# Kernel tuning notes

Measured on AMD Instinct MI355X. Metric: run time of the kernel, lower is better.

Reference implementation:

```python
import jax, jax.numpy as jnp
import numpy as np
from jax import lax

EPS = 1e-8
QB = 127.0  # 2**(8-1) - 1
LN_EPS = 1e-5

B, S, E, D = 32, 4096, 64, 32


def _ste(x, q):
    return x + lax.stop_gradient(q - x)


def _bitlinear(x, w, b):
    # BitLinear158b: ternary absmean weight quant + 8-bit absmax activation quant (STE)
    beta = jnp.maximum(jnp.mean(jnp.abs(w)), EPS)
    wq = jnp.clip(jnp.round(w / beta), -1.0, 1.0) * beta
    gamma = QB / jnp.maximum(jnp.max(jnp.abs(x), axis=-1, keepdims=True), EPS)
    xq = jnp.clip(jnp.round(x * gamma), -(QB + 1.0), QB) / gamma
    return _ste(x, xq) @ _ste(w, wq).T + b


def _layernorm(x, g, b):
    m = jnp.mean(x, axis=-1, keepdims=True)
    v = jnp.mean(jnp.square(x - m), axis=-1, keepdims=True)
    return (x - m) * lax.rsqrt(v + LN_EPS) * g + b


def _conv3x3(x, w, b):
    y = lax.conv_general_dilated(x, w, (1, 1), 'SAME',
                                 dimension_numbers=('NCHW', 'OIHW', 'NCHW'))
    return y + b.reshape(1, -1, 1, 1)


def _gelu(x):
    return jax.nn.gelu(x, approximate=False)


def setup_inputs() -> dict:
    key = jax.random.key(0)
    ks = jax.random.split(key, 20)
    d = {
        'x': jax.random.normal(ks[0], (B, S, E), jnp.float32),
        'interact2': jax.random.normal(ks[1], (B, D, D), jnp.float32),
        'qw': jax.random.normal(ks[2], (E, E), jnp.float32) * 0.05,
        'qb': jnp.zeros((E,), jnp.float32),
        'kw': jax.random.normal(ks[3], (E, E), jnp.float32) * 0.05,
        'kb': jnp.zeros((E,), jnp.float32),
        'vw': jax.random.normal(ks[4], (E, E), jnp.float32) * 0.05,
        'vb': jnp.zeros((E,), jnp.float32),
        'f1w': jax.random.normal(ks[5], (E, E), jnp.float32) * 0.05,
        'f1b': jnp.zeros((E,), jnp.float32),
        'f2w': jax.random.normal(ks[6], (E, E), jnp.float32) * 0.05,
        'f2b': jnp.zeros((E,), jnp.float32),
        'c1w': jax.random.normal(ks[7], (1, 1, 3, 3), jnp.float32) * 0.2,
        'c1b': jnp.zeros((1,), jnp.float32),
        'c2w': jax.random.normal(ks[8], (1, 1, 3, 3), jnp.float32) * 0.2,
        'c2b': jnp.zeros((1,), jnp.float32),
        'c3w': jax.random.normal(ks[9], (1, 1, 3, 3), jnp.float32) * 0.2,
        'c3b': jnp.zeros((1,), jnp.float32),
        'ln1g': jnp.ones((E,), jnp.float32), 'ln1b': jnp.zeros((E,), jnp.float32),
        'ln2g': jnp.ones((E,), jnp.float32), 'ln2b': jnp.zeros((E,), jnp.float32),
        'ln3g': jnp.ones((E,), jnp.float32), 'ln3b': jnp.zeros((E,), jnp.float32),
        'ln4g': jnp.ones((E,), jnp.float32), 'ln4b': jnp.zeros((E,), jnp.float32),
    }
    return d


def reference(x, interact2, qw, qb, kw, kb, vw, vb, f1w, f1b, f2w, f2b,
              c1w, c1b, c2w, c2b, c3w, c3b,
              ln1g, ln1b, ln2g, ln2b, ln3g, ln3b, ln4g, ln4b):
    residual1 = x
    b, s, e = x.shape
    xn = _layernorm(x, ln1g, ln1b)
    # NOTE: .view(B, E, S) is a raw reinterpret of the (B,S,E) buffer, not a transpose
    q = _bitlinear(xn, qw, qb).reshape(b, e, s)
    k = _bitlinear(xn, kw, kb).reshape(b, e, s)
    v = _bitlinear(xn, vw, vb).reshape(b, e, s)

    it = interact2[:, None, :, :]
    it = jax.image.resize(it, (b, 1, 64, 64), method='linear')  # align_corners=False
    it = _gelu(_conv3x3(it, c1w, c1b))  # dropout4: identity (eval)
    it = _gelu(_conv3x3(it, c2w, c2b))
    it = _gelu(_conv3x3(it, c3w, c3b))
    it = it[:, 0]  # (B, 64, 64)

    scale = jnp.sqrt(jnp.float32(e))
    scores = jnp.einsum('bes,bfs->bef', q, k) / scale + it  # (B,E,E)
    attn = jax.nn.softmax(scores, axis=-1)
    out = jnp.einsum('bef,bfs->bes', attn, v)  # (B,E,S)
    out = jnp.transpose(out, (0, 2, 1)).reshape(b, s, e)
    out = out - xn  # dropout: identity (eval)
    out = _layernorm(out, ln2g, ln2b)
    residual2 = out + residual1
    out = _layernorm(out + residual1, ln3g, ln3b)
    out = _gelu(_bitlinear(out, f1w, f1b))
    out = _layernorm(out, ln4g, ln4b)
    out = _bitlinear(out, f2w, f2b)
    return out + residual2
```

## Files before the change

### kernel.cpp

```cpp
#include <hip/hip_runtime.h>

#define EPSQ 1e-8f
#define QBC  127.0f
#define LNE  1e-5f

#if defined(__has_builtin)
#  if __has_builtin(__builtin_amdgcn_sdot4)
#    define SDOT4(a,b,c) __builtin_amdgcn_sdot4((a),(b),(c),false)
#  endif
#endif
#ifndef SDOT4
__device__ __forceinline__ int sdot4_sw(int a, int b, int c){
  c += ((a<<24)>>24) * ((b<<24)>>24);
  c += ((a<<16)>>24) * ((b<<16)>>24);
  c += ((a<< 8)>>24) * ((b<< 8)>>24);
  c += ( a>>24     ) * ( b>>24     );
  return c;
}
#  define SDOT4(a,b,c) sdot4_sw((a),(b),(c))
#endif

constexpr size_t OFF_WPK  = 0;
constexpr size_t OFF_BETA = 20480;
constexpr size_t OFF_IG   = 20544;
constexpr size_t OFF_XN   = OFF_IG + 524288;
constexpr size_t OFF_Q    = OFF_XN + 33554432;
constexpr size_t OFF_K    = OFF_Q  + 16777216;
constexpr size_t OFF_V    = OFF_K  + 16777216;
constexpr size_t OFF_SC   = OFF_V  + 16777216;
constexpr size_t OFF_AT   = OFF_SC + 524288;

__device__ __forceinline__ float gelu_f(float v){
  return 0.5f * v * (1.0f + erff(v * 0.70710678118654752f));
}
__device__ __forceinline__ int pack4(float q0, float q1, float q2, float q3){
  return ((int)q0 & 255) | (((int)q1 & 255) << 8) | (((int)q2 & 255) << 16) | (((int)q3 & 255) << 24);
}

__global__ __launch_bounds__(256) void k_prep(
    const float* qw, const float* kw, const float* vw, const float* f1w, const float* f2w,
    const float* it2, const float* c1w, const float* c1b, const float* c2w, const float* c2b,
    const float* c3w, const float* c3b, int* __restrict__ wpk, float* __restrict__ beta5,
    float* __restrict__ sco){
  __shared__ float smem[1024 + 2*64*65];
  int t = threadIdx.x;
  if (blockIdx.x < 5){
    int m = blockIdx.x;
    const float* w = (m==0)?qw:(m==1)?kw:(m==2)?vw:(m==3)?f1w:f2w;
    float* red = smem;
    float s = 0.f;
    for (int i = t; i < 4096; i += 256) s += fabsf(w[i]);
    red[t] = s; __syncthreads();
    for (int o = 128; o > 0; o >>= 1){ if (t < o) red[t] += red[t+o]; __syncthreads(); }
    float beta = fmaxf(red[0] * (1.0f/4096.0f), EPSQ);
    if (t == 0) beta5[m] = beta;
    int* dst = wpk + m*1024;
    for (int idx = t; idx < 1024; idx += 256){
      int row = idx >> 4, kp = idx & 15;
      int v = 0;
      #pragma unroll
      for (int j = 0; j < 4; j++){
        float q = rintf(w[row*64 + kp*4 + j] / beta);
        q = fminf(fmaxf(q, -1.f), 1.f);
        v |= ((int)q & 255) << (8*j);
      }
      dst[idx] = v;
    }
  } else {
    int b = blockIdx.x - 5;
    float* in32 = smem;
    float (*Aa)[65] = (float(*)[65])(smem + 1024);
    float (*Bb)[65] = (float(*)[65])(smem + 1024 + 64*65);
    for (int i = t; i < 1024; i += 256) in32[i] = it2[b*1024 + i];
    __syncthreads();
    for (int p = t; p < 4096; p += 256){
      int i = p >> 6, j = p & 63;
      float si = 0.5f*i - 0.25f, fi = floorf(si), wi = si - fi;
      int i0 = min(max((int)fi, 0), 31), i1 = min(max((int)fi + 1, 0), 31);
      float sj = 0.5f*j - 0.25f, fj = floorf(sj), wj = sj - fj;
      int j0 = min(max((int)fj, 0), 31), j1 = min(max((int)fj + 1, 0), 31);
      float v00 = in32[i0*32+j0], v01 = in32[i0*32+j1];
      float v10 = in32[i1*32+j0], v11 = in32[i1*32+j1];
      Aa[i][j] = (1.f-wi)*((1.f-wj)*v00 + wj*v01) + wi*((1.f-wj)*v10 + wj*v11);
    }
    __syncthreads();
    {
      float w9[9]; for (int q2=0;q2<9;q2++) w9[q2]=c1w[q2]; float bb = c1b[0];
      for (int p = t; p < 4096; p += 256){
        int i = p>>6, j = p&63; float s = bb;
        #pragma unroll
        for (int di=-1; di<=1; di++)
          #pragma unroll
          for (int dj=-1; dj<=1; dj++){
            int ii=i+di, jj=j+dj;
            if (ii>=0 && ii<64 && jj>=0 && jj<64) s += w9[(di+1)*3+dj+1]*Aa[ii][jj];
          }
        Bb[i][j] = gelu_f(s);
      }
    }
    __syncthreads();
    {
      float w9[9]; for (int q2=0;q2<9;q2++) w9[q2]=c2w[q2]; float bb = c2b[0];
      for (int p = t; p < 4096; p += 256){
        int i = p>>6, j = p&63; float s = bb;
        #pragma unroll
        for (int di=-1; di<=1; di++)
          #pragma unroll
          for (int dj=-1; dj<=1; dj++){
            int ii=i+di, jj=j+dj;
            if (ii>=0 && ii<64 && jj>=0 && jj<64) s += w9[(di+1)*3+dj+1]*Bb[ii][jj];
          }
        Aa[i][j] = gelu_f(s);
      }
    }
    __syncthreads();
    {
      float w9[9]; for (int q2=0;q2<9;q2++) w9[q2]=c3w[q2]; float bb = c3b[0];
      for (int p = t; p < 4096; p += 256){
        int i = p>>6, j = p&63; float s = bb;
        #pragma unroll
        for (int di=-1; di<=1; di++)
          #pragma unroll
          for (int dj=-1; dj<=1; dj++){
            int ii=i+di, jj=j+dj;
            if (ii>=0 && ii<64 && jj>=0 && jj<64) s += w9[(di+1)*3+dj+1]*Aa[ii][jj];
          }
        sco[b*4096 + p] = gelu_f(s);
      }
    }
  }
}

__global__ __launch_bounds__(256,4) void k_qkv(const float* __restrict__ x,
    const float* __restrict__ ln1g, const float* __restrict__ ln1b,
    const int* __restrict__ wpk, float* __restrict__ xn, float* __restrict__ ig,
    short* __restrict__ q16, short* __restrict__ k16, short* __restrict__ v16){
  __shared__ int Wp[3][64][17];
  __shared__ int Xp[64][17];
  int t = threadIdx.x;
  for (int i = t; i < 3072; i += 256){
    int m = i >> 10, rem = i & 1023;
    Wp[m][rem>>4][rem&15] = wpk[i];
  }
  int c = t >> 2, g = t & 3;
  long n = (long)blockIdx.x * 64 + c;
  const float* xr = x + n*64 + g*16;
  float xv[16];
  #pragma unroll
  for (int i4 = 0; i4 < 4; i4++){
    float4 f = ((const float4*)xr)[i4];
    xv[4*i4+0]=f.x; xv[4*i4+1]=f.y; xv[4*i4+2]=f.z; xv[4*i4+3]=f.w;
  }
  float s = 0.f;
  #pragma unroll
  for (int i = 0; i < 16; i++) s += xv[i];
  s += __shfl_xor(s,1); s += __shfl_xor(s,2);
  float mean = s * (1.0f/64.0f);
  float vs = 0.f;
  #pragma unroll
  for (int i = 0; i < 16; i++){ float dd = xv[i]-mean; vs += dd*dd; }
  vs += __shfl_xor(vs,1); vs += __shfl_xor(vs,2);
  float rs = rsqrtf(vs*(1.0f/64.0f) + LNE);
  float xnv[16]; float amax = 0.f;
  #pragma unroll
  for (int i = 0; i < 16; i++){
    float u = (xv[i]-mean)*rs*ln1g[g*16+i] + ln1b[g*16+i];
    xnv[i] = u; amax = fmaxf(amax, fabsf(u));
  }
  float* xnp = xn + n*64 + g*16;
  #pragma unroll
  for (int i4 = 0; i4 < 4; i4++)
    ((float4*)xnp)[i4] = make_float4(xnv[4*i4],xnv[4*i4+1],xnv[4*i4+2],xnv[4*i4+3]);
  amax = fmaxf(amax, __shfl_xor(amax,1)); amax = fmaxf(amax, __shfl_xor(amax,2));
  float am = fmaxf(amax, EPSQ);
  float gamma = QBC / am;
  if (g == 0) ig[n] = am * (1.0f/QBC);
  #pragma unroll
  for (int i4 = 0; i4 < 4; i4++){
    float q0 = fminf(fmaxf(rintf(xnv[4*i4+0]*gamma), -128.f), 127.f);
    float q1 = fminf(fmaxf(rintf(xnv[4*i4+1]*gamma), -128.f), 127.f);
    float q2 = fminf(fmaxf(rintf(xnv[4*i4+2]*gamma), -128.f), 127.f);
    float q3 = fminf(fmaxf(rintf(xnv[4*i4+3]*gamma), -128.f), 127.f);
    Xp[c][g*4+i4] = pack4(q0,q1,q2,q3);
  }
  __syncthreads();

  int r0 = (t >> 4) << 2, c0 = (t & 15) << 2;
  #pragma unroll
  for (int m = 0; m < 3; m++){
    int acc[4][4] = {};
    #pragma unroll
    for (int kp = 0; kp < 16; kp++){
      int av[4], bv[4];
      #pragma unroll
      for (int i = 0; i < 4; i++) av[i] = Xp[r0+i][kp];
      #pragma unroll
      for (int j = 0; j < 4; j++) bv[j] = Wp[m][c0+j][kp];
      #pragma unroll
      for (int i = 0; i < 4; i++)
        #pragma unroll
        for (int j = 0; j < 4; j++)
          acc[i][j] = SDOT4(av[i], bv[j], acc[i][j]);
    }
    short* op = ((m==0)?q16:(m==1)?k16:v16) + (long)blockIdx.x*4096;
    #pragma unroll
    for (int i = 0; i < 4; i++){
      short4 s4;
      s4.x = (short)acc[i][0]; s4.y = (short)acc[i][1];
      s4.z = (short)acc[i][2]; s4.w = (short)acc[i][3];
      *(short4*)&op[(r0+i)*64 + c0] = s4;
    }
  }
}

__global__ __launch_bounds__(256,4) void k_qk(
    const short* __restrict__ q16, const short* __restrict__ k16,
    const float* __restrict__ ig, const float* __restrict__ beta5,
    const float* __restrict__ qbias, const float* __restrict__ kbias,
    float* __restrict__ sco){
  __shared__ float Qs[64][68];
  __shared__ float Kt[64][68];
  __shared__ float qbs[64], kbs[64];
  int t = threadIdx.x;
  int b = blockIdx.x >> 4, ch = blockIdx.x & 15;
  int c = t >> 2, g = t & 3;
  int r0 = (t >> 4) << 2, c0 = (t & 15) << 2;
  if (t < 64){ qbs[t] = qbias[t]; kbs[t] = kbias[t]; }
  float bq = beta5[0], bk = beta5[1];
  const short* qbase = q16 + (long)b*262144 + (long)c*4096;
  const short* kbase = k16 + (long)b*262144 + (long)c*4096;
  float acc[4][4] = {};
  for (int sub = 0; sub < 4; sub++){
    int t0 = ch*256 + sub*64 + g*16;
    int4 qa = *(const int4*)(qbase + t0);
    int4 qb2 = *(const int4*)(qbase + t0 + 8);
    int4 ka = *(const int4*)(kbase + t0);
    int4 kb2 = *(const int4*)(kbase + t0 + 8);
    float sgi = ig[b*4096 + c*64 + ch*4 + sub];
    float sq = bq * sgi, sk = bk * sgi;
    __syncthreads();
    int qi[8] = {qa.x,qa.y,qa.z,qa.w,qb2.x,qb2.y,qb2.z,qb2.w};
    int ki[8] = {ka.x,ka.y,ka.z,ka.w,kb2.x,kb2.y,kb2.z,kb2.w};
    #pragma unroll
    for (int w2 = 0; w2 < 8; w2++){
      int e0 = g*16 + 2*w2, e1 = e0 + 1;
      Qs[c][e0] = (float)((qi[w2]<<16)>>16)*sq + qbs[e0];
      Qs[c][e1] = (float)( qi[w2]>>16      )*sq + qbs[e1];
      Kt[e0][c] = (float)((ki[w2]<<16)>>16)*sk + kbs[e0];
      Kt[e1][c] = (float)( ki[w2]>>16      )*sk + kbs[e1];
    }
    __syncthreads();
    for (int k4 = 0; k4 < 64; k4 += 4){
      float4 a[4], bv[4];
      #pragma unroll
      for (int i = 0; i < 4; i++) a[i] = *(const float4*)&Qs[r0+i][k4];
      #pragma unroll
      for (int kk = 0; kk < 4; kk++) bv[kk] = *(const float4*)&Kt[k4+kk][c0];
      #pragma unroll
      for (int i = 0; i < 4; i++){
        const float* ap = (const float*)&a[i];
        #pragma unroll
        for (int kk = 0; kk < 4; kk++){
          float av = ap[kk];
          acc[i][0] = fmaf(av, bv[kk].x, acc[i][0]);
          acc[i][1] = fmaf(av, bv[kk].y, acc[i][1]);
          acc[i][2] = fmaf(av, bv[kk].z, acc[i][2]);
          acc[i][3] = fmaf(av, bv[kk].w, acc[i][3]);
        }
      }
    }
  }
  float* sc = sco + b*4096;
  #pragma unroll
  for (int i = 0; i < 4; i++)
    #pragma unroll
    for (int j = 0; j < 4; j++)
      atomicAdd(&sc[(r0+i)*64 + c0 + j], acc[i][j]*0.125f);
}

__global__ __launch_bounds__(256) void k_smax(const float* __restrict__ sco, float* __restrict__ at){
  int row = blockIdx.x*4 + (threadIdx.x >> 6);
  int lane = threadIdx.x & 63;
  float v = sco[row*64 + lane];
  float m = v;
  #pragma unroll
  for (int o = 1; o < 64; o <<= 1) m = fmaxf(m, __shfl_xor(m, o));
  float e = expf(v - m);
  float s = e;
  #pragma unroll
  for (int o = 1; o < 64; o <<= 1) s += __shfl_xor(s, o);
  at[row*64 + lane] = e / s;
}

__global__ __launch_bounds__(256,3) void k_epi(const float* __restrict__ x,
    const short* __restrict__ v16, const float* __restrict__ at,
    const float* __restrict__ xn, const float* __restrict__ ig,
    const float* __restrict__ beta5, const int* __restrict__ wpk,
    const float* ln2g, const float* ln2b, const float* ln3g, const float* ln3b,
    const float* ln4g, const float* ln4b, const float* __restrict__ vbias,
    const float* f1b, const float* f2b, float* __restrict__ out){
  __shared__ float B1[64][68];
  __shared__ float B2[64][68];
  __shared__ int Wp[2][64][17];
  __shared__ int Xp[64][17];
  __shared__ float gam1[64], gam2[64];
  int t = threadIdx.x;
  int b = blockIdx.x >> 6;
  int s0 = (blockIdx.x & 63) << 6;
  float bv_ = beta5[2];
  for (int i = t; i < 4096; i += 256){
    int r = i >> 6, cc = i & 63;
    B1[r][cc] = at[b*4096 + i];
    float sv = bv_ * ig[b*4096 + r*64 + (s0 >> 6)];
    B2[r][cc] = (float)v16[(long)b*262144 + (long)r*4096 + s0 + cc] * sv + vbias[cc];
  }
  for (int i = t; i < 2048; i += 256){
    int m = i >> 10, rem = i & 1023;
    Wp[m][rem>>4][rem&15] = wpk[(3+m)*1024 + rem];
  }
  __syncthreads();
  int r0 = (t >> 4) << 2, c0 = (t & 15) << 2;
  float acc[4][4] = {};
  for (int k4 = 0; k4 < 64; k4 += 4){
    float4 a[4], bv[4];
    #pragma unroll
    for (int i = 0; i < 4; i++) a[i] = *(const float4*)&B1[r0+i][k4];
    #pragma unroll
    for (int kk = 0; kk < 4; kk++) bv[kk] = *(const float4*)&B2[k4+kk][c0];
    #pragma unroll
    for (int i = 0; i < 4; i++){
      const float* ap = (const float*)&a[i];
      #pragma unroll
      for (int kk = 0; kk < 4; kk++){
        float av = ap[kk];
        acc[i][0] = fmaf(av, bv[kk].x, acc[i][0]);
        acc[i][1] = fmaf(av, bv[kk].y, acc[i][1]);
        acc[i][2] = fmaf(av, bv[kk].z, acc[i][2]);
        acc[i][3] = fmaf(av, bv[kk].w, acc[i][3]);
      }
    }
  }
  __syncthreads();
  #pragma unroll
  for (int i = 0; i < 4; i++)
    #pragma unroll
    for (int j = 0; j < 4; j++) B1[c0+j][r0+i] = acc[i][j];
  __syncthreads();
  int c = t >> 2, g = t & 3;
  long n = (long)b*4096 + s0 + c;
  float d[16];
  #pragma unroll
  for (int i4 = 0; i4 < 4; i4++){
    float4 f = *(const float4*)&B1[c][g*16 + 4*i4];
    d[4*i4+0]=f.x; d[4*i4+1]=f.y; d[4*i4+2]=f.z; d[4*i4+3]=f.w;
  }
  const float* xnp = xn + n*64 + g*16;
  #pragma unroll
  for (int i4 = 0; i4 < 4; i4++){
    float4 f = ((const float4*)xnp)[i4];
    d[4*i4+0]-=f.x; d[4*i4+1]-=f.y; d[4*i4+2]-=f.z; d[4*i4+3]-=f.w;
  }
  float s = 0.f;
  #pragma unroll
  for (int i = 0; i < 16; i++) s += d[i];
  s += __shfl_xor(s,1); s += __shfl_xor(s,2);
  float mean = s*(1.0f/64.0f);
  float vs = 0.f;
  #pragma unroll
  for (int i = 0; i < 16; i++){ float dd = d[i]-mean; vs += dd*dd; }
  vs += __shfl_xor(vs,1); vs += __shfl_xor(vs,2);
  float rs = rsqrtf(vs*(1.0f/64.0f) + LNE);
  const float* xp = x + n*64 + g*16;
  float r2[16];
  #pragma unroll
  for (int i4 = 0; i4 < 4; i4++){
    float4 xf = ((const float4*)xp)[i4];
    float xa[4] = {xf.x, xf.y, xf.z, xf.w};
    #pragma unroll
    for (int q2 = 0; q2 < 4; q2++){
      int i = 4*i4+q2;
      float t2 = (d[i]-mean)*rs*ln2g[g*16+i] + ln2b[g*16+i];
      r2[i] = t2 + xa[q2];
    }
  }
  #pragma unroll
  for (int i4 = 0; i4 < 4; i4++)
    *(float4*)&B2[c][g*16+4*i4] = make_float4(r2[4*i4],r2[4*i4+1],r2[4*i4+2],r2[4*i4+3]);
  s = 0.f;
  #pragma unroll
  for (int i = 0; i < 16; i++) s += r2[i];
  s += __shfl_xor(s,1); s += __shfl_xor(s,2);
  float mean3 = s*(1.0f/64.0f);
  vs = 0.f;
  #pragma unroll
  for (int i = 0; i < 16; i++){ float dd = r2[i]-mean3; vs += dd*dd; }
  vs += __shfl_xor(vs,1); vs += __shfl_xor(vs,2);
  float rs3 = rsqrtf(vs*(1.0f/64.0f) + LNE);
  float u16v[16]; float amax = 0.f;
  #pragma unroll
  for (int i = 0; i < 16; i++){
    float u = (r2[i]-mean3)*rs3*ln3g[g*16+i] + ln3b[g*16+i];
    u16v[i] = u; amax = fmaxf(amax, fabsf(u));
  }
  amax = fmaxf(amax, __shfl_xor(amax,1)); amax = fmaxf(amax, __shfl_xor(amax,2));
  float gamma = QBC / fmaxf(amax, EPSQ);
  #pragma unroll
  for (int i4 = 0; i4 < 4; i4++){
    float q0 = fminf(fmaxf(rintf(u16v[4*i4+0]*gamma), -128.f), 127.f);
    float q1 = fminf(fmaxf(rintf(u16v[4*i4+1]*gamma), -128.f), 127.f);
    float q2 = fminf(fmaxf(rintf(u16v[4*i4+2]*gamma), -128.f), 127.f);
    float q3 = fminf(fmaxf(rintf(u16v[4*i4+3]*gamma), -128.f), 127.f);
    Xp[c][g*4+i4] = pack4(q0,q1,q2,q3);
  }
  if (g == 0) gam1[c] = gamma;
  __syncthreads();
  int ac2[4][4] = {};
  #pragma unroll
  for (int kp = 0; kp < 16; kp++){
    int av[4], bv2[4];
    #pragma unroll
    for (int i = 0; i < 4; i++) av[i] = Xp[r0+i][kp];
    #pragma unroll
    for (int j = 0; j < 4; j++) bv2[j] = Wp[0][c0+j][kp];
    #pragma unroll
    for (int i = 0; i < 4; i++)
      #pragma unroll
      for (int j = 0; j < 4; j++)
        ac2[i][j] = SDOT4(av[i], bv2[j], ac2[i][j]);
  }
  __syncthreads();
  float beta1 = beta5[3], beta2 = beta5[4];
  #pragma unroll
  for (int i = 0; i < 4; i++){
    float sc = beta1 / gam1[r0+i];
    #pragma unroll
    for (int j = 0; j < 4; j++)
      B1[r0+i][c0+j] = gelu_f((float)ac2[i][j]*sc + f1b[c0+j]);
  }
  __syncthreads();
  float gl[16];
  #pragma unroll
  for (int i4 = 0; i4 < 4; i4++){
    float4 f = *(const float4*)&B1[c][g*16 + 4*i4];
    gl[4*i4+0]=f.x; gl[4*i4+1]=f.y; gl[4*i4+2]=f.z; gl[4*i4+3]=f.w;
  }
  s = 0.f;
  #pragma unroll
  for (int i = 0; i < 16; i++) s += gl[i];
  s += __shfl_xor(s,1); s += __shfl_xor(s,2);
  float mean4 = s*(1.0f/64.0f);
  vs = 0.f;
  #pragma unroll
  for (int i = 0; i < 16; i++){ float dd = gl[i]-mean4; vs += dd*dd; }
  vs += __shfl_xor(vs,1); vs += __shfl_xor(vs,2);
  float rs4 = rsqrtf(vs*(1.0f/64.0f) + LNE);
  amax = 0.f;
  #pragma unroll
  for (int i = 0; i < 16; i++){
    float u = (gl[i]-mean4)*rs4*ln4g[g*16+i] + ln4b[g*16+i];
    u16v[i] = u; amax = fmaxf(amax, fabsf(u));
  }
  amax = fmaxf(amax, __shfl_xor(amax,1)); amax = fmaxf(amax, __shfl_xor(amax,2));
  float gamma2 = QBC / fmaxf(amax, EPSQ);
  #pragma unroll
  for (int i4 = 0; i4 < 4; i4++){
    float q0 = fminf(fmaxf(rintf(u16v[4*i4+0]*gamma2), -128.f), 127.f);
    float q1 = fminf(fmaxf(rintf(u16v[4*i4+1]*gamma2), -128.f), 127.f);
    float q2 = fminf(fmaxf(rintf(u16v[4*i4+2]*gamma2), -128.f), 127.f);
    float q3 = fminf(fmaxf(rintf(u16v[4*i4+3]*gamma2), -128.f), 127.f);
    Xp[c][g*4+i4] = pack4(q0,q1,q2,q3);
  }
  if (g == 0) gam2[c] = gamma2;
  __syncthreads();
  int ac3[4][4] = {};
  #pragma unroll
  for (int kp = 0; kp < 16; kp++){
    int av[4], bv2[4];
    #pragma unroll
    for (int i = 0; i < 4; i++) av[i] = Xp[r0+i][kp];
    #pragma unroll
    for (int j = 0; j < 4; j++) bv2[j] = Wp[1][c0+j][kp];
    #pragma unroll
    for (int i = 0; i < 4; i++)
      #pragma unroll
      for (int j = 0; j < 4; j++)
        ac3[i][j] = SDOT4(av[i], bv2[j], ac3[i][j]);
  }
  float4 bf = *(const float4*)&f2b[c0];
  #pragma unroll
  for (int i = 0; i < 4; i++){
    float sc = beta2 / gam2[r0+i];
    float4 rr = *(const float4*)&B2[r0+i][c0];
    float4 o = make_float4((float)ac3[i][0]*sc + bf.x + rr.x, (float)ac3[i][1]*sc + bf.y + rr.y,
                           (float)ac3[i][2]*sc + bf.z + rr.z, (float)ac3[i][3]*sc + bf.w + rr.w);
    *(float4*)&out[((long)b*4096 + s0 + r0 + i)*64 + c0] = o;
  }
}

extern "C" void kernel_launch(void* const* d_in, const int* in_sizes, int n_in,
                              void* d_out, int out_size, void* d_ws, size_t ws_size,
                              hipStream_t stream){
  const float* x    = (const float*)d_in[0];
  const float* it2  = (const float*)d_in[1];
  const float* qw   = (const float*)d_in[2];
  const float* qb   = (const float*)d_in[3];
  const float* kw   = (const float*)d_in[4];
  const float* kb   = (const float*)d_in[5];
  const float* vw   = (const float*)d_in[6];
  const float* vb   = (const float*)d_in[7];
  const float* f1w  = (const float*)d_in[8];
  const float* f1b  = (const float*)d_in[9];
  const float* f2w  = (const float*)d_in[10];
  const float* f2b  = (const float*)d_in[11];
  const float* c1w  = (const float*)d_in[12];
  const float* c1b  = (const float*)d_in[13];
  const float* c2w  = (const float*)d_in[14];
  const float* c2b  = (const float*)d_in[15];
  const float* c3w  = (const float*)d_in[16];
  const float* c3b  = (const float*)d_in[17];
  const float* ln1g = (const float*)d_in[18];
  const float* ln1b = (const float*)d_in[19];
  const float* ln2g = (const float*)d_in[20];
  const float* ln2b = (const float*)d_in[21];
  const float* ln3g = (const float*)d_in[22];
  const float* ln3b = (const float*)d_in[23];
  const float* ln4g = (const float*)d_in[24];
  const float* ln4b = (const float*)d_in[25];
  float* out = (float*)d_out;

  char* w = (char*)d_ws;
  int*   wpk   = (int*)(w + OFF_WPK);
  float* beta5 = (float*)(w + OFF_BETA);
  float* ig    = (float*)(w + OFF_IG);
  float* xn    = (float*)(w + OFF_XN);
  short* q16   = (short*)(w + OFF_Q);
  short* k16   = (short*)(w + OFF_K);
  short* v16   = (short*)(w + OFF_V);
  float* sco   = (float*)(w + OFF_SC);
  float* at    = (float*)(w + OFF_AT);

  hipLaunchKernelGGL(k_prep, dim3(37),   dim3(256), 0, stream,
                     qw, kw, vw, f1w, f2w, it2, c1w, c1b, c2w, c2b, c3w, c3b, wpk, beta5, sco);
  hipLaunchKernelGGL(k_qkv,  dim3(2048), dim3(256), 0, stream,
                     x, ln1g, ln1b, wpk, xn, ig, q16, k16, v16);
  hipLaunchKernelGGL(k_qk,   dim3(512),  dim3(256), 0, stream,
                     q16, k16, ig, beta5, qb, kb, sco);
  hipLaunchKernelGGL(k_smax, dim3(512),  dim3(256), 0, stream, sco, at);
  hipLaunchKernelGGL(k_epi,  dim3(2048), dim3(256), 0, stream,
                     x, v16, at, xn, ig, beta5, wpk,
                     ln2g, ln2b, ln3g, ln3b, ln4g, ln4b, vb, f1b, f2b, out);
}
```

Measured before the change: 320.1 us.

## Recompute LN1 output in epilogue, fuse softmax, widen prep and qk grids

```diff
diff --git a/kernel.cpp b/kernel.cpp
--- a/kernel.cpp
+++ b/kernel.cpp
@@ -3,6 +3,8 @@
 #define EPSQ 1e-8f
 #define QBC  127.0f
 #define LNE  1e-5f
+
+typedef float f32x4 __attribute__((ext_vector_type(4)));
 
 #if defined(__has_builtin)
 #  if __has_builtin(__builtin_amdgcn_sdot4)
@@ -23,12 +25,11 @@
 constexpr size_t OFF_WPK  = 0;
 constexpr size_t OFF_BETA = 20480;
 constexpr size_t OFF_IG   = 20544;
-constexpr size_t OFF_XN   = OFF_IG + 524288;
-constexpr size_t OFF_Q    = OFF_XN + 33554432;
+constexpr size_t OFF_MR   = OFF_IG + 524288;
+constexpr size_t OFF_Q    = OFF_MR + 1048576;
 constexpr size_t OFF_K    = OFF_Q  + 16777216;
 constexpr size_t OFF_V    = OFF_K  + 16777216;
 constexpr size_t OFF_SC   = OFF_V  + 16777216;
-constexpr size_t OFF_AT   = OFF_SC + 524288;
 
 __device__ __forceinline__ float gelu_f(float v){
   return 0.5f * v * (1.0f + erff(v * 0.70710678118654752f));
@@ -37,7 +38,7 @@
   return ((int)q0 & 255) | (((int)q1 & 255) << 8) | (((int)q2 & 255) << 16) | (((int)q3 & 255) << 24);
 }
 
-__global__ __launch_bounds__(256) void k_prep(
+__global__ __launch_bounds__(1024) void k_prep(
     const float* qw, const float* kw, const float* vw, const float* f1w, const float* f2w,
     const float* it2, const float* c1w, const float* c1b, const float* c2w, const float* c2b,
     const float* c3w, const float* c3b, int* __restrict__ wpk, float* __restrict__ beta5,
@@ -49,14 +50,14 @@
     const float* w = (m==0)?qw:(m==1)?kw:(m==2)?vw:(m==3)?f1w:f2w;
     float* red = smem;
     float s = 0.f;
-    for (int i = t; i < 4096; i += 256) s += fabsf(w[i]);
+    for (int i = t; i < 4096; i += 1024) s += fabsf(w[i]);
     red[t] = s; __syncthreads();
-    for (int o = 128; o > 0; o >>= 1){ if (t < o) red[t] += red[t+o]; __syncthreads(); }
+    for (int o = 512; o > 0; o >>= 1){ if (t < o) red[t] += red[t+o]; __syncthreads(); }
     float beta = fmaxf(red[0] * (1.0f/4096.0f), EPSQ);
     if (t == 0) beta5[m] = beta;
     int* dst = wpk + m*1024;
-    for (int idx = t; idx < 1024; idx += 256){
-      int row = idx >> 4, kp = idx & 15;
+    if (t < 1024){
+      int row = t >> 4, kp = t & 15;
       int v = 0;
       #pragma unroll
       for (int j = 0; j < 4; j++){
@@ -64,16 +65,16 @@
         q = fminf(fmaxf(q, -1.f), 1.f);
         v |= ((int)q & 255) << (8*j);
       }
-      dst[idx] = v;
+      dst[t] = v;
     }
   } else {
     int b = blockIdx.x - 5;
     float* in32 = smem;
     float (*Aa)[65] = (float(*)[65])(smem + 1024);
     float (*Bb)[65] = (float(*)[65])(smem + 1024 + 64*65);
-    for (int i = t; i < 1024; i += 256) in32[i] = it2[b*1024 + i];
+    for (int i = t; i < 1024; i += 1024) in32[i] = it2[b*1024 + i];
     __syncthreads();
-    for (int p = t; p < 4096; p += 256){
+    for (int p = t; p < 4096; p += 1024){
       int i = p >> 6, j = p & 63;
       float si = 0.5f*i - 0.25f, fi = floorf(si), wi = si - fi;
       int i0 = min(max((int)fi, 0), 31), i1 = min(max((int)fi + 1, 0), 31);
@@ -86,7 +87,7 @@
     __syncthreads();
     {
       float w9[9]; for (int q2=0;q2<9;q2++) w9[q2]=c1w[q2]; float bb = c1b[0];
-      for (int p = t; p < 4096; p += 256){
+      for (int p = t; p < 4096; p += 1024){
         int i = p>>6, j = p&63; float s = bb;
         #pragma unroll
         for (int di=-1; di<=1; di++)
@@ -101,7 +102,7 @@
     __syncthreads();
     {
       float w9[9]; for (int q2=0;q2<9;q2++) w9[q2]=c2w[q2]; float bb = c2b[0];
-      for (int p = t; p < 4096; p += 256){
+      for (int p = t; p < 4096; p += 1024){
         int i = p>>6, j = p&63; float s = bb;
         #pragma unroll
         for (int di=-1; di<=1; di++)
@@ -116,7 +117,7 @@
     __syncthreads();
     {
       float w9[9]; for (int q2=0;q2<9;q2++) w9[q2]=c3w[q2]; float bb = c3b[0];
-      for (int p = t; p < 4096; p += 256){
+      for (int p = t; p < 4096; p += 1024){
         int i = p>>6, j = p&63; float s = bb;
         #pragma unroll
         for (int di=-1; di<=1; di++)
@@ -131,9 +132,9 @@
   }
 }
 
-__global__ __launch_bounds__(256,4) void k_qkv(const float* __restrict__ x,
+__global__ __launch_bounds__(256,8) void k_qkv(const float* __restrict__ x,
     const float* __restrict__ ln1g, const float* __restrict__ ln1b,
-    const int* __restrict__ wpk, float* __restrict__ xn, float* __restrict__ ig,
+    const int* __restrict__ wpk, float2* __restrict__ mr, float* __restrict__ ig,
     short* __restrict__ q16, short* __restrict__ k16, short* __restrict__ v16){
   __shared__ int Wp[3][64][17];
   __shared__ int Xp[64][17];
@@ -167,14 +168,10 @@
     float u = (xv[i]-mean)*rs*ln1g[g*16+i] + ln1b[g*16+i];
     xnv[i] = u; amax = fmaxf(amax, fabsf(u));
   }
-  float* xnp = xn + n*64 + g*16;
-  #pragma unroll
-  for (int i4 = 0; i4 < 4; i4++)
-    ((float4*)xnp)[i4] = make_float4(xnv[4*i4],xnv[4*i4+1],xnv[4*i4+2],xnv[4*i4+3]);
   amax = fmaxf(amax, __shfl_xor(amax,1)); amax = fmaxf(amax, __shfl_xor(amax,2));
   float am = fmaxf(amax, EPSQ);
   float gamma = QBC / am;
-  if (g == 0) ig[n] = am * (1.0f/QBC);
+  if (g == 0){ ig[n] = am * (1.0f/QBC); mr[n] = make_float2(mean, rs); }
   #pragma unroll
   for (int i4 = 0; i4 < 4; i4++){
     float q0 = fminf(fmaxf(rintf(xnv[4*i4+0]*gamma), -128.f), 127.f);
@@ -222,7 +219,7 @@
   __shared__ float Kt[64][68];
   __shared__ float qbs[64], kbs[64];
   int t = threadIdx.x;
-  int b = blockIdx.x >> 4, ch = blockIdx.x & 15;
+  int b = blockIdx.x >> 5, ch = blockIdx.x & 31;
   int c = t >> 2, g = t & 3;
   int r0 = (t >> 4) << 2, c0 = (t & 15) << 2;
   if (t < 64){ qbs[t] = qbias[t]; kbs[t] = kbias[t]; }
@@ -230,13 +227,13 @@
   const short* qbase = q16 + (long)b*262144 + (long)c*4096;
   const short* kbase = k16 + (long)b*262144 + (long)c*4096;
   float acc[4][4] = {};
-  for (int sub = 0; sub < 4; sub++){
-    int t0 = ch*256 + sub*64 + g*16;
+  for (int sub = 0; sub < 2; sub++){
+    int t0 = ch*128 + sub*64 + g*16;
     int4 qa = *(const int4*)(qbase + t0);
     int4 qb2 = *(const int4*)(qbase + t0 + 8);
     int4 ka = *(const int4*)(kbase + t0);
     int4 kb2 = *(const int4*)(kbase + t0 + 8);
-    float sgi = ig[b*4096 + c*64 + ch*4 + sub];
+    float sgi = ig[b*4096 + c*64 + ch*2 + sub];
     float sq = bq * sgi, sk = bk * sgi;
     __syncthreads();
     int qi[8] = {qa.x,qa.y,qa.z,qa.w,qb2.x,qb2.y,qb2.z,qb2.w};
@@ -278,24 +275,11 @@
       atomicAdd(&sc[(r0+i)*64 + c0 + j], acc[i][j]*0.125f);
 }
 
-__global__ __launch_bounds__(256) void k_smax(const float* __restrict__ sco, float* __restrict__ at){
-  int row = blockIdx.x*4 + (threadIdx.x >> 6);
-  int lane = threadIdx.x & 63;
-  float v = sco[row*64 + lane];
-  float m = v;
-  #pragma unroll
-  for (int o = 1; o < 64; o <<= 1) m = fmaxf(m, __shfl_xor(m, o));
-  float e = expf(v - m);
-  float s = e;
-  #pragma unroll
-  for (int o = 1; o < 64; o <<= 1) s += __shfl_xor(s, o);
-  at[row*64 + lane] = e / s;
-}
-
 __global__ __launch_bounds__(256,3) void k_epi(const float* __restrict__ x,
-    const short* __restrict__ v16, const float* __restrict__ at,
-    const float* __restrict__ xn, const float* __restrict__ ig,
+    const short* __restrict__ v16, const float* __restrict__ sco,
+    const float2* __restrict__ mr, const float* __restrict__ ig,
     const float* __restrict__ beta5, const int* __restrict__ wpk,
+    const float* ln1g, const float* ln1b,
     const float* ln2g, const float* ln2b, const float* ln3g, const float* ln3b,
     const float* ln4g, const float* ln4b, const float* __restrict__ vbias,
     const float* f1b, const float* f2b, float* __restrict__ out){
@@ -310,13 +294,35 @@
   float bv_ = beta5[2];
   for (int i = t; i < 4096; i += 256){
     int r = i >> 6, cc = i & 63;
-    B1[r][cc] = at[b*4096 + i];
+    B1[r][cc] = sco[b*4096 + i];
     float sv = bv_ * ig[b*4096 + r*64 + (s0 >> 6)];
     B2[r][cc] = (float)v16[(long)b*262144 + (long)r*4096 + s0 + cc] * sv + vbias[cc];
   }
   for (int i = t; i < 2048; i += 256){
     int m = i >> 10, rem = i & 1023;
     Wp[m][rem>>4][rem&15] = wpk[(3+m)*1024 + rem];
+  }
+  __syncthreads();
+  int c = t >> 2, g = t & 3;
+  {
+    float sv[16];
+    #pragma unroll
+    for (int i4 = 0; i4 < 4; i4++){
+      float4 f = *(const float4*)&B1[c][g*16 + 4*i4];
+      sv[4*i4+0]=f.x; sv[4*i4+1]=f.y; sv[4*i4+2]=f.z; sv[4*i4+3]=f.w;
+    }
+    float mx = sv[0];
+    #pragma unroll
+    for (int i = 1; i < 16; i++) mx = fmaxf(mx, sv[i]);
+    mx = fmaxf(mx, __shfl_xor(mx,1)); mx = fmaxf(mx, __shfl_xor(mx,2));
+    float se = 0.f;
+    #pragma unroll
+    for (int i = 0; i < 16; i++){ sv[i] = expf(sv[i]-mx); se += sv[i]; }
+    se += __shfl_xor(se,1); se += __shfl_xor(se,2);
+    float inv = 1.0f/se;
+    #pragma unroll
+    for (int i4 = 0; i4 < 4; i4++)
+      *(float4*)&B1[c][g*16+4*i4] = make_float4(sv[4*i4]*inv, sv[4*i4+1]*inv, sv[4*i4+2]*inv, sv[4*i4+3]*inv);
   }
   __syncthreads();
   int r0 = (t >> 4) << 2, c0 = (t & 15) << 2;
@@ -346,19 +352,25 @@
     #pragma unroll
     for (int j = 0; j < 4; j++) B1[c0+j][r0+i] = acc[i][j];
   __syncthreads();
-  int c = t >> 2, g = t & 3;
   long n = (long)b*4096 + s0 + c;
+  const float* xp = x + n*64 + g*16;
+  float xa[16];
+  #pragma unroll
+  for (int i4 = 0; i4 < 4; i4++){
+    float4 f = ((const float4*)xp)[i4];
+    xa[4*i4+0]=f.x; xa[4*i4+1]=f.y; xa[4*i4+2]=f.z; xa[4*i4+3]=f.w;
+  }
+  float2 m2 = mr[n];
   float d[16];
   #pragma unroll
   for (int i4 = 0; i4 < 4; i4++){
     float4 f = *(const float4*)&B1[c][g*16 + 4*i4];
     d[4*i4+0]=f.x; d[4*i4+1]=f.y; d[4*i4+2]=f.z; d[4*i4+3]=f.w;
   }
-  const float* xnp = xn + n*64 + g*16;
-  #pragma unroll
-  for (int i4 = 0; i4 < 4; i4++){
-    float4 f = ((const float4*)xnp)[i4];
-    d[4*i4+0]-=f.x; d[4*i4+1]-=f.y; d[4*i4+2]-=f.z; d[4*i4+3]-=f.w;
+  #pragma unroll
+  for (int i = 0; i < 16; i++){
+    float xn_i = (xa[i]-m2.x)*m2.y*ln1g[g*16+i] + ln1b[g*16+i];
+    d[i] -= xn_i;
   }
   float s = 0.f;
   #pragma unroll
@@ -370,18 +382,11 @@
   for (int i = 0; i < 16; i++){ float dd = d[i]-mean; vs += dd*dd; }
   vs += __shfl_xor(vs,1); vs += __shfl_xor(vs,2);
   float rs = rsqrtf(vs*(1.0f/64.0f) + LNE);
-  const float* xp = x + n*64 + g*16;
   float r2[16];
   #pragma unroll
-  for (int i4 = 0; i4 < 4; i4++){
-    float4 xf = ((const float4*)xp)[i4];
-    float xa[4] = {xf.x, xf.y, xf.z, xf.w};
-    #pragma unroll
-    for (int q2 = 0; q2 < 4; q2++){
-      int i = 4*i4+q2;
-      float t2 = (d[i]-mean)*rs*ln2g[g*16+i] + ln2b[g*16+i];
-      r2[i] = t2 + xa[q2];
-    }
+  for (int i = 0; i < 16; i++){
+    float t2 = (d[i]-mean)*rs*ln2g[g*16+i] + ln2b[g*16+i];
+    r2[i] = t2 + xa[i];
   }
   #pragma unroll
   for (int i4 = 0; i4 < 4; i4++)
@@ -491,9 +496,12 @@
   for (int i = 0; i < 4; i++){
     float sc = beta2 / gam2[r0+i];
     float4 rr = *(const float4*)&B2[r0+i][c0];
-    float4 o = make_float4((float)ac3[i][0]*sc + bf.x + rr.x, (float)ac3[i][1]*sc + bf.y + rr.y,
-                           (float)ac3[i][2]*sc + bf.z + rr.z, (float)ac3[i][3]*sc + bf.w + rr.w);
-    *(float4*)&out[((long)b*4096 + s0 + r0 + i)*64 + c0] = o;
+    f32x4 o;
+    o.x = (float)ac3[i][0]*sc + bf.x + rr.x;
+    o.y = (float)ac3[i][1]*sc + bf.y + rr.y;
+    o.z = (float)ac3[i][2]*sc + bf.z + rr.z;
+    o.w = (float)ac3[i][3]*sc + bf.w + rr.w;
+    __builtin_nontemporal_store(o, (f32x4*)&out[((long)b*4096 + s0 + r0 + i)*64 + c0]);
   }
 }
 
@@ -529,24 +537,22 @@
   float* out = (float*)d_out;
 
   char* w = (char*)d_ws;
-  int*   wpk   = (int*)(w + OFF_WPK);
-  float* beta5 = (float*)(w + OFF_BETA);
-  float* ig    = (float*)(w + OFF_IG);
-  float* xn    = (float*)(w + OFF_XN);
-  short* q16   = (short*)(w + OFF_Q);
-  short* k16   = (short*)(w + OFF_K);
-  short* v16   = (short*)(w + OFF_V);
-  float* sco   = (float*)(w + OFF_SC);
-  float* at    = (float*)(w + OFF_AT);
-
-  hipLaunchKernelGGL(k_prep, dim3(37),   dim3(256), 0, stream,
+  int*    wpk   = (int*)(w + OFF_WPK);
+  float*  beta5 = (float*)(w + OFF_BETA);
+  float*  ig    = (float*)(w + OFF_IG);
+  float2* mr    = (float2*)(w + OFF_MR);
+  short*  q16   = (short*)(w + OFF_Q);
+  short*  k16   = (short*)(w + OFF_K);
+  short*  v16   = (short*)(w + OFF_V);
+  float*  sco   = (float*)(w + OFF_SC);
+
+  hipLaunchKernelGGL(k_prep, dim3(37),   dim3(1024), 0, stream,
                      qw, kw, vw, f1w, f2w, it2, c1w, c1b, c2w, c2b, c3w, c3b, wpk, beta5, sco);
   hipLaunchKernelGGL(k_qkv,  dim3(2048), dim3(256), 0, stream,
-                     x, ln1g, ln1b, wpk, xn, ig, q16, k16, v16);
-  hipLaunchKernelGGL(k_qk,   dim3(512),  dim3(256), 0, stream,
+                     x, ln1g, ln1b, wpk, mr, ig, q16, k16, v16);
+  hipLaunchKernelGGL(k_qk,   dim3(1024), dim3(256), 0, stream,
                      q16, k16, ig, beta5, qb, kb, sco);
-  hipLaunchKernelGGL(k_smax, dim3(512),  dim3(256), 0, stream, sco, at);
   hipLaunchKernelGGL(k_epi,  dim3(2048), dim3(256), 0, stream,
-                     x, v16, at, xn, ig, beta5, wpk,
+                     x, v16, sco, mr, ig, beta5, wpk, ln1g, ln1b,
                      ln2g, ln2b, ln3g, ln3b, ln4g, ln4b, vb, f1b, f2b, out);
 }
```

Result: slower. 410.0 us (+28.1%).
